# Optimization experiments

Measured on AMD Instinct MI355X. Metric: run time of the kernel, lower is better.

Reference implementation:

```python
import jax, jax.numpy as jnp
import numpy as np

B, NQ, NC, C, NH, NP, DFF, HH, WW = 4, 300, 16, 256, 8, 4, 2048, 128, 128


def _ln(x, g, b):
    m = jnp.mean(x, -1, keepdims=True)
    v = jnp.mean((x - m) ** 2, -1, keepdims=True)
    return (x - m) / jnp.sqrt(v + 1e-5) * g + b


def _mha(x, wi, bi, wo, bo, n_heads):
    Bx, L, Cx = x.shape
    d = Cx // n_heads
    q, k, v = jnp.split(x @ wi.T + bi, 3, axis=-1)
    sh = lambda t: t.reshape(Bx, L, n_heads, d).transpose(0, 2, 1, 3)
    scale = float(1.0 / np.sqrt(d))
    a = jax.nn.softmax(jnp.einsum('bhqd,bhkd->bhqk', sh(q), sh(k)) * scale, axis=-1)
    o = jnp.einsum('bhqk,bhkd->bhqd', a, sh(v)).transpose(0, 2, 1, 3).reshape(Bx, L, Cx)
    return o @ wo.T + bo


def _grid_sample(im, grid):
    # im: [N, Ch, H, W]; grid: [N, L, P, 2] in [-1,1]; bilinear, zeros padding, align_corners=False
    N, Ch, H, W = im.shape
    gx = (grid[..., 0] + 1.0) * (W * 0.5) - 0.5
    gy = (grid[..., 1] + 1.0) * (H * 0.5) - 0.5
    x0 = jnp.floor(gx)
    y0 = jnp.floor(gy)
    wx1 = gx - x0
    wy1 = gy - y0
    imf = im.reshape(N, Ch, H * W)

    def gather(xi, yi):
        valid = ((xi >= 0) & (xi < W) & (yi >= 0) & (yi < H)).astype(im.dtype)
        idx = jnp.clip(yi, 0, H - 1).astype(jnp.int32) * W + jnp.clip(xi, 0, W - 1).astype(jnp.int32)
        vals = jnp.take_along_axis(imf, idx.reshape(N, 1, -1), axis=2).reshape(N, Ch, *xi.shape[1:])
        return vals * valid[:, None]

    return (gather(x0, y0) * ((1 - wx1) * (1 - wy1))[:, None]
            + gather(x0 + 1, y0) * (wx1 * (1 - wy1))[:, None]
            + gather(x0, y0 + 1) * ((1 - wx1) * wy1)[:, None]
            + gather(x0 + 1, y0 + 1) * (wx1 * wy1)[:, None])


def setup_inputs() -> dict:
    key = jax.random.key(0)
    ks = jax.random.split(key, 30)
    s = 0.02
    p = lambda k, shp: jax.random.normal(k, shp, jnp.float32) * s
    cxcy = jax.random.uniform(ks[0], (B, NQ * NC, 2), jnp.float32)
    wh = jax.random.uniform(ks[1], (B, NQ * NC, 2), jnp.float32) * 0.2 + 0.02
    return {
        'inst_query': jax.random.normal(ks[2], (B, NQ, C), jnp.float32),
        'sub_contour_query': jax.random.normal(ks[3], (B, NQ, NC, C), jnp.float32),
        'memory_feats': jax.random.normal(ks[4], (B, HH * WW, C), jnp.float32),
        'reference_boxes': jnp.concatenate([cxcy, wh], axis=-1),
        'inst_in_w': p(ks[5], (3 * C, C)), 'inst_in_b': p(ks[6], (3 * C,)),
        'inst_out_w': p(ks[7], (C, C)), 'inst_out_b': p(ks[8], (C,)),
        'sc_in_w': p(ks[9], (3 * C, C)), 'sc_in_b': p(ks[10], (3 * C,)),
        'sc_out_w': p(ks[11], (C, C)), 'sc_out_b': p(ks[12], (C,)),
        'off_w': p(ks[13], (NH * NP * 2, C)), 'off_b': p(ks[14], (NH * NP * 2,)),
        'aw_w': p(ks[15], (NH * NP, C)), 'aw_b': p(ks[16], (NH * NP,)),
        'outp_w': p(ks[17], (C, C)), 'outp_b': p(ks[18], (C,)),
        'lin1_w': p(ks[19], (DFF, C)), 'lin1_b': p(ks[20], (DFF,)),
        'lin2_w': p(ks[21], (C, DFF)), 'lin2_b': p(ks[22], (C,)),
        'n1_g': jnp.ones((C,), jnp.float32), 'n1_b': jnp.zeros((C,), jnp.float32),
        'n2_g': jnp.ones((C,), jnp.float32), 'n2_b': jnp.zeros((C,), jnp.float32),
        'n3_g': jnp.ones((C,), jnp.float32), 'n3_b': jnp.zeros((C,), jnp.float32),
        'H': HH, 'W': WW,
    }


def reference(inst_query, sub_contour_query, memory_feats, reference_boxes,
              inst_in_w, inst_in_b, inst_out_w, inst_out_b,
              sc_in_w, sc_in_b, sc_out_w, sc_out_b,
              off_w, off_b, aw_w, aw_b, outp_w, outp_b,
              lin1_w, lin1_b, lin2_w, lin2_b,
              n1_g, n1_b, n2_g, n2_b, n3_g, n3_b, H, W):
    Bx, Nq, Nc, Cx = sub_contour_query.shape
    Lq = Nq * Nc
    hd = Cx // NH
    # --- decoupled self-attention (eval mode: dropout = identity) ---
    inst_o = _mha(inst_query, inst_in_w, inst_in_b, inst_out_w, inst_out_b, NH)
    sc = sub_contour_query.transpose(0, 2, 1, 3).reshape(Bx * Nc, Nq, Cx)
    sc_o = _mha(sc, sc_in_w, sc_in_b, sc_out_w, sc_out_b, NH)
    sc_o = sc_o.reshape(Bx, Nc, Nq, Cx).transpose(0, 2, 1, 3)
    q_sa = sc_o + inst_o[:, :, None, :]
    tgt = (sub_contour_query + q_sa).reshape(Bx, Lq, Cx)
    tgt = _ln(tgt + q_sa.reshape(Bx, Lq, Cx), n1_g, n1_b)
    # --- deformable cross-attention ---
    offsets = (tgt @ off_w.T + off_b).reshape(Bx, Lq, NH, NP, 2)
    aw = jax.nn.softmax((tgt @ aw_w.T + aw_b).reshape(Bx, Lq, NH, NP), axis=-1)
    ref = reference_boxes[:, :, None, None, :]
    loc = ref[..., :2] + offsets * ref[..., 2:] * 0.5
    grid = (loc * 2.0 - 1.0).transpose(0, 2, 1, 3, 4).reshape(Bx * NH, Lq, NP, 2)
    mem = memory_feats.reshape(Bx, H, W, Cx).transpose(0, 3, 1, 2).reshape(Bx * NH, hd, H, W)
    samp = _grid_sample(mem, grid).reshape(Bx, NH, hd, Lq, NP).transpose(0, 3, 1, 4, 2)  # [B,Lq,nH,nP,hd]
    tgt2 = (samp * aw[..., None]).sum(3).reshape(Bx, Lq, Cx) @ outp_w.T + outp_b
    tgt = _ln(tgt + tgt2, n2_g, n2_b)
    # --- FFN ---
    tgt2 = jax.nn.relu(tgt @ lin1_w.T + lin1_b) @ lin2_w.T + lin2_b
    tgt = _ln(tgt + tgt2, n3_g, n3_b)
    return tgt.reshape(Bx, Nq, Nc, Cx)
```

## Files before the change

### kernel.cpp

```cpp
#include <hip/hip_runtime.h>
#include <hip/hip_bf16.h>
#include <math.h>


typedef unsigned short u16;
typedef unsigned int u32;
typedef __attribute__((ext_vector_type(4))) float f32x4;
typedef __attribute__((ext_vector_type(8))) short s16x8;

__device__ __forceinline__ float b2f(u16 u) {
    union { u32 u; float f; } v; v.u = ((u32)u) << 16; return v.f;
}
__device__ __forceinline__ u16 f2b(float f) {
    union { float f; u32 u; } v; v.f = f;
    u32 r = v.u + 0x7fffu + ((v.u >> 16) & 1u);
    return (u16)(r >> 16);
}
__device__ __forceinline__ u32 pkbf(float a, float b) {
    u32 r;
    asm("v_cvt_pk_bf16_f32 %0, %1, %2" : "=v"(r) : "v"(a), "v"(b));
    return r;
}

#define GLOAD_LDS16(g, l) \
    __builtin_amdgcn_global_load_lds((const __attribute__((address_space(1))) void*)(g), \
                                     (__attribute__((address_space(3))) void*)(l), 16, 0, 0)

struct CvtSeg { const float* src; u16* dst; int nv; };
struct Cvt8 { CvtSeg s[8]; };

__global__ __launch_bounds__(256) void cvt_multi(Cvt8 a, int totalv) {
    int v = blockIdx.x * 256 + threadIdx.x;
    if (v >= totalv) return;
    int si = 0;
    while (si < 7 && v >= a.s[si].nv) { v -= a.s[si].nv; ++si; }
    const float* src = a.s[si].src + (size_t)v * 8;
    u16* dst = a.s[si].dst + (size_t)v * 8;
    float4 x = *(const float4*)src;
    float4 y = *(const float4*)(src + 4);
    u16 u[8] = { f2b(x.x), f2b(x.y), f2b(x.z), f2b(x.w),
                 f2b(y.x), f2b(y.y), f2b(y.z), f2b(y.w) };
    *(uint4*)dst = *(const uint4*)u;
}

__global__ __launch_bounds__(256) void pack_offaw(
    const float* __restrict__ off_w, const float* __restrict__ off_b,
    const float* __restrict__ aw_w, const float* __restrict__ aw_b,
    u16* __restrict__ wout, float* __restrict__ bout)
{
    int r = blockIdx.x, c = threadIdx.x;
    float v = 0.f;
    if (r < 64) v = off_w[r * 256 + c];
    else if (r < 96) v = aw_w[(r - 64) * 256 + c];
    wout[r * 256 + c] = f2b(v);
    if (c == 0) bout[r] = (r < 64) ? off_b[r] : (r < 96 ? aw_b[r - 64] : 0.f);
}

template<int RELU, int OUTBF16, int TM>
__global__ __launch_bounds__(256) void gemm_mfma(
    const u16* __restrict__ A, const u16* __restrict__ W,
    const float* __restrict__ bias, void* __restrict__ Cout,
    int M, int N, int K)
{
    constexpr int MI = TM / 32;
    constexpr int AU = TM / 64;
    __shared__ u16 smem[TM * 32 + 128 * 32];
    u16* Asm = smem;
    u16* Bsm = smem + TM * 32;
    const int tid = threadIdx.x;
    const int wave = tid >> 6, lane = tid & 63;
    const int bm = blockIdx.y * TM, bn = blockIdx.x * 128;
    const int wr = (wave >> 1) * (TM / 2), wc = (wave & 1) * 64;
    const int fr = lane & 15;
    const int fk = (lane >> 4) * 8;
    f32x4 acc[MI][4] = {};

    for (int k0 = 0; k0 < K; k0 += 32) {
        __syncthreads();
#pragma unroll
        for (int c = 0; c < AU; ++c) {
            int b = (c * 256 + tid) * 16;
            int row = b >> 6;
            int ke = (b & 63) >> 1;
            int ra = bm + row; if (ra >= M) ra = M - 1;
            GLOAD_LDS16(A + (size_t)ra * K + k0 + ke, Asm + (c * 256 + wave * 64) * 8);
        }
#pragma unroll
        for (int c = 0; c < 2; ++c) {
            int b = (c * 256 + tid) * 16;
            int row = b >> 6;
            int ke = (b & 63) >> 1;
            int rb = bn + row;
            GLOAD_LDS16(W + (size_t)rb * K + k0 + ke, Bsm + (c * 256 + wave * 64) * 8);
        }
        __syncthreads();
        s16x8 af[MI], bf[4];
#pragma unroll
        for (int i = 0; i < MI; ++i)
            af[i] = *(const s16x8*)(Asm + (wr + i * 16 + fr) * 32 + fk);
#pragma unroll
        for (int i = 0; i < 4; ++i)
            bf[i] = *(const s16x8*)(Bsm + (wc + i * 16 + fr) * 32 + fk);
#pragma unroll
        for (int mi = 0; mi < MI; ++mi)
#pragma unroll
            for (int ni = 0; ni < 4; ++ni)
                acc[mi][ni] = __builtin_amdgcn_mfma_f32_16x16x32_bf16(
                    af[mi], bf[ni], acc[mi][ni], 0, 0, 0);
    }
    const int cc = lane & 15, cr4 = (lane >> 4) * 4;
    if (OUTBF16) {
#pragma unroll
        for (int p = 0; p < TM / 32; ++p) {
            const int base = p * 32;
            __syncthreads();
#pragma unroll
            for (int mi = 0; mi < MI; ++mi) {
                int rowoff = wr + mi * 16;
                if (rowoff < base || rowoff >= base + 32) continue;
#pragma unroll
                for (int ni = 0; ni < 4; ++ni) {
                    int col = wc + ni * 16 + cc;
                    float bv = bias[bn + col];
#pragma unroll
                    for (int j = 0; j < 4; ++j) {
                        float v = acc[mi][ni][j] + bv;
                        if (RELU) v = fmaxf(v, 0.f);
                        smem[(rowoff - base + cr4 + j) * 136 + col] = f2b(v);
                    }
                }
            }
            __syncthreads();
            for (int t = tid; t < 512; t += 256) {
                int row = t >> 4, ck = t & 15;
                int grow = bm + base + row;
                if (grow < M)
                    *(uint4*)((u16*)Cout + (size_t)grow * N + bn + ck * 8) =
                        *(const uint4*)&smem[row * 136 + ck * 8];
            }
        }
    } else {
#pragma unroll
        for (int mi = 0; mi < MI; ++mi) {
#pragma unroll
            for (int ni = 0; ni < 4; ++ni) {
                int col = bn + wc + ni * 16 + cc;
                float bv = bias[col];
#pragma unroll
                for (int j = 0; j < 4; ++j) {
                    int row = bm + wr + mi * 16 + cr4 + j;
                    if (row >= M) continue;
                    float v = acc[mi][ni][j] + bv;
                    if (RELU) v = fmaxf(v, 0.f);
                    ((float*)Cout)[(size_t)row * N + col] = v;
                }
            }
        }
    }
}

#define VIDX(d, k) ((((k) >> 3) ^ ((d) & 7)) * 8 + ((k) & 7))

__global__ __launch_bounds__(256) void attn_mfma(
    const u16* __restrict__ qkv, u16* __restrict__ O, int S)
{
    const int bh = blockIdx.x / S, seg = blockIdx.x % S;
    const int bi = bh >> 3, h = bh & 7;
    __shared__ u16 Ks[320][40];
    __shared__ u16 Vt[32][384];
    const int tid = threadIdx.x;

    for (int idx = tid; idx < 1200; idx += 256) {
        int k = idx >> 2, sub = idx & 3;
        const u16* kp = qkv + ((size_t)(bi * 300 + k)) * 768 + 256 + h * 32 + sub * 8;
        *(uint4*)&Ks[k][sub * 8] = *(const uint4*)kp;
    }
    for (int idx = tid; idx < 600; idx += 256) {
        int kp2 = idx >> 2, sub = idx & 3;
        int k0 = kp2 * 2;
        const u16* vp = qkv + ((size_t)(bi * 300 + k0)) * 768 + 512 + h * 32 + sub * 8;
        uint4 v0 = *(const uint4*)vp;
        uint4 v1 = *(const uint4*)(vp + 768);
        u16 a0[8], a1[8];
        *(uint4*)a0 = v0; *(uint4*)a1 = v1;
#pragma unroll
        for (int j = 0; j < 8; ++j) {
            int d = sub * 8 + j;
            *(u32*)&Vt[d][VIDX(d, k0)] = (u32)a0[j] | ((u32)a1[j] << 16);
        }
    }
    for (int idx = tid; idx < 320; idx += 256) {
        int d = idx & 31, k0 = 300 + (idx >> 5) * 2;
        *(u32*)&Vt[d][VIDX(d, k0)] = 0;
    }
    __syncthreads();

    const int lane = tid & 63, wave = tid >> 6;
    const int c = lane & 15, g = lane >> 4;
    const int fk = g * 8;
    const f32x4 zero = { 0.f, 0.f, 0.f, 0.f };
    const float SCL2 = 0.25505416f;
    const int sA = c + ((g & 1) << 5);
    const int sB = sA + 16;
    const bool hi = g >= 2;

    for (int qt = seg * 4 + wave; qt < 19; qt += 4 * S) {
        int qrow = qt * 16 + c; if (qrow > 299) qrow = 299;
        s16x8 afq = *(const s16x8*)(qkv + ((size_t)(bi * 300 + qrow)) * 768 + h * 32 + fk);
        f32x4 acc0 = zero, acc1 = zero;
        float m = -1e30f, l = 0.f;

        for (int kc = 0; kc < 10; ++kc) {
            const int kb = kc * 32;
            s16x8 ak0 = *(const s16x8*)&Ks[kb + c][fk];
            s16x8 ak1 = *(const s16x8*)&Ks[kb + 16 + c][fk];
            __builtin_amdgcn_s_setprio(1);
            f32x4 s0 = __builtin_amdgcn_mfma_f32_16x16x32_bf16(ak0, afq, zero, 0, 0, 0);
            f32x4 s1 = __builtin_amdgcn_mfma_f32_16x16x32_bf16(ak1, afq, zero, 0, 0, 0);
            __builtin_amdgcn_s_setprio(0);
            if (kb == 288) {
#pragma unroll
                for (int j = 0; j < 4; ++j) {
                    if (g == 3) s0[j] = -1e30f;
                    s1[j] = -1e30f;
                }
            }
            float cm = fmaxf(fmaxf(fmaxf(s0[0], s0[1]), fmaxf(s0[2], s0[3])),
                             fmaxf(fmaxf(s1[0], s1[1]), fmaxf(s1[2], s1[3])));
            cm = fmaxf(cm, __shfl_xor(cm, 16));
            cm = fmaxf(cm, __shfl_xor(cm, 32));
            float mn = fmaxf(m, cm);
            float corr = exp2f((m - mn) * SCL2);
            m = mn;
            float p0[4], p1[4];
#pragma unroll
            for (int j = 0; j < 4; ++j) {
                p0[j] = exp2f((s0[j] - m) * SCL2);
                p1[j] = exp2f((s1[j] - m) * SCL2);
            }
            float cs = (p0[0] + p0[1]) + (p0[2] + p0[3])
                     + (p1[0] + p1[1]) + (p1[2] + p1[3]);
            cs += __shfl_xor(cs, 16);
            cs += __shfl_xor(cs, 32);
            l = l * corr + cs;
            u32 w0 = pkbf(p0[0], p0[1]), w1 = pkbf(p0[2], p0[3]);
            u32 w2 = pkbf(p1[0], p1[1]), w3 = pkbf(p1[2], p1[3]);
            int x0 = __shfl((int)w0, sA), x1 = __shfl((int)w1, sA);
            int x2 = __shfl((int)w2, sA), x3 = __shfl((int)w3, sA);
            int y0 = __shfl((int)w0, sB), y1 = __shfl((int)w1, sB);
            int y2 = __shfl((int)w2, sB), y3 = __shfl((int)w3, sB);
            union { u32 w[4]; s16x8 v; } afp;
            afp.w[0] = hi ? (u32)x2 : (u32)x0;
            afp.w[1] = hi ? (u32)x3 : (u32)x1;
            afp.w[2] = hi ? (u32)y2 : (u32)y0;
            afp.w[3] = hi ? (u32)y3 : (u32)y1;
            float c0 = __shfl(corr, g * 4 + 0), c1 = __shfl(corr, g * 4 + 1);
            float c2 = __shfl(corr, g * 4 + 2), c3 = __shfl(corr, g * 4 + 3);
            acc0[0] *= c0; acc0[1] *= c1; acc0[2] *= c2; acc0[3] *= c3;
            acc1[0] *= c0; acc1[1] *= c1; acc1[2] *= c2; acc1[3] *= c3;
            s16x8 bv0 = *(const s16x8*)&Vt[c][VIDX(c, kb + fk)];
            s16x8 bv1 = *(const s16x8*)&Vt[16 + c][VIDX(16 + c, kb + fk)];
            __builtin_amdgcn_s_setprio(1);
            acc0 = __builtin_amdgcn_mfma_f32_16x16x32_bf16(afp.v, bv0, acc0, 0, 0, 0);
            acc1 = __builtin_amdgcn_mfma_f32_16x16x32_bf16(afp.v, bv1, acc1, 0, 0, 0);
            __builtin_amdgcn_s_setprio(0);
        }
        float l0 = __shfl(l, g * 4 + 0), l1 = __shfl(l, g * 4 + 1);
        float l2 = __shfl(l, g * 4 + 2), l3 = __shfl(l, g * 4 + 3);
        float lj[4] = { l0, l1, l2, l3 };
#pragma unroll
        for (int j = 0; j < 4; ++j) {
            int q = qt * 16 + g * 4 + j;
            if (q < 300) {
                float r = 1.f / lj[j];
                u16* op = O + ((size_t)(bi * 300 + q)) * 256 + h * 32;
                op[c]      = f2b(acc0[j] * r);
                op[16 + c] = f2b(acc1[j] * r);
            }
        }
    }
}

__global__ __launch_bounds__(256) void sc_transpose(
    const float* __restrict__ scq, u16* __restrict__ out)
{
    int row = blockIdx.x * 4 + (threadIdx.x >> 6);
    int c4 = (threadIdx.x & 63) * 4;
    int b = row / 4800;
    int rem = row % 4800;
    int nc = rem / 300, nq = rem % 300;
    float4 v = *(const float4*)(scq + ((size_t)((b * 300 + nq) * 16 + nc)) * 256 + c4);
    u16 u[4] = { f2b(v.x), f2b(v.y), f2b(v.z), f2b(v.w) };
    *(uint2*)(out + (size_t)row * 256 + c4) = *(const uint2*)u;
}

__global__ __launch_bounds__(256) void ln1_combine(
    const float* __restrict__ scq, const float* __restrict__ sco,
    const float* __restrict__ insto, const float* __restrict__ g,
    const float* __restrict__ bta, float* __restrict__ tgt,
    u16* __restrict__ tgtb)
{
    int row = blockIdx.x * 4 + (threadIdx.x >> 6);
    int c4 = (threadIdx.x & 63) * 4;
    int b = row / 4800;
    int rem = row % 4800;
    int nq = rem >> 4, nc = rem & 15;
    float4 a = *(const float4*)(scq + (size_t)row * 256 + c4);
    float4 s = *(const float4*)(sco + ((size_t)((b * 16 + nc) * 300 + nq)) * 256 + c4);
    float4 i = *(const float4*)(insto + ((size_t)(b * 300 + nq)) * 256 + c4);
    float4 v = { a.x + 2.f * (s.x + i.x), a.y + 2.f * (s.y + i.y),
                 a.z + 2.f * (s.z + i.z), a.w + 2.f * (s.w + i.w) };
    float sm = v.x + v.y + v.z + v.w;
    float s2 = v.x * v.x + v.y * v.y + v.z * v.z + v.w * v.w;
#pragma unroll
    for (int o = 32; o; o >>= 1) { sm += __shfl_xor(sm, o); s2 += __shfl_xor(s2, o); }
    float mean = sm * (1.f / 256.f);
    float rstd = 1.f / sqrtf(s2 * (1.f / 256.f) - mean * mean + 1e-5f);
    float4 gv = *(const float4*)(g + c4);
    float4 bv = *(const float4*)(bta + c4);
    float4 r = { (v.x - mean) * rstd * gv.x + bv.x, (v.y - mean) * rstd * gv.y + bv.y,
                 (v.z - mean) * rstd * gv.z + bv.z, (v.w - mean) * rstd * gv.w + bv.w };
    *(float4*)(tgt + (size_t)row * 256 + c4) = r;
    u16 u[4] = { f2b(r.x), f2b(r.y), f2b(r.z), f2b(r.w) };
    *(uint2*)(tgtb + (size_t)row * 256 + c4) = *(const uint2*)u;
}

__global__ __launch_bounds__(256) void ln_add(
    const float* __restrict__ x, const float* __restrict__ y,
    const float* __restrict__ g, const float* __restrict__ bta,
    float* __restrict__ dst, u16* __restrict__ bdst)
{
    int row = blockIdx.x * 4 + (threadIdx.x >> 6);
    int c4 = (threadIdx.x & 63) * 4;
    float4 a = *(const float4*)(x + (size_t)row * 256 + c4);
    float4 b = *(const float4*)(y + (size_t)row * 256 + c4);
    float4 v = { a.x + b.x, a.y + b.y, a.z + b.z, a.w + b.w };
    float sm = v.x + v.y + v.z + v.w;
    float s2 = v.x * v.x + v.y * v.y + v.z * v.z + v.w * v.w;
#pragma unroll
    for (int o = 32; o; o >>= 1) { sm += __shfl_xor(sm, o); s2 += __shfl_xor(s2, o); }
    float mean = sm * (1.f / 256.f);
    float rstd = 1.f / sqrtf(s2 * (1.f / 256.f) - mean * mean + 1e-5f);
    float4 gv = *(const float4*)(g + c4);
    float4 bv = *(const float4*)(bta + c4);
    float4 r = { (v.x - mean) * rstd * gv.x + bv.x, (v.y - mean) * rstd * gv.y + bv.y,
                 (v.z - mean) * rstd * gv.z + bv.z, (v.w - mean) * rstd * gv.w + bv.w };
    *(float4*)(dst + (size_t)row * 256 + c4) = r;
    if (bdst) {
        u16 u[4] = { f2b(r.x), f2b(r.y), f2b(r.z), f2b(r.w) };
        *(uint2*)(bdst + (size_t)row * 256 + c4) = *(const uint2*)u;
    }
}

__global__ __launch_bounds__(256) void deform_sample(
    const float* __restrict__ oaw, const float* __restrict__ refb,
    const float* __restrict__ mem, u16* __restrict__ samp)
{
    const int row = blockIdx.x;
    const int b = row / 4800;
    const int tid = threadIdx.x;
    const int h = tid >> 5;
    const float4 rb = *(const float4*)(refb + (size_t)row * 4);
    const float* base = oaw + (size_t)row * 128;
    float a0 = base[64 + h * 4 + 0], a1 = base[64 + h * 4 + 1];
    float a2 = base[64 + h * 4 + 2], a3 = base[64 + h * 4 + 3];
    float am = fmaxf(fmaxf(a0, a1), fmaxf(a2, a3));
    float e0 = __expf(a0 - am), e1 = __expf(a1 - am), e2 = __expf(a2 - am), e3 = __expf(a3 - am);
    float rs = 1.f / (e0 + e1 + e2 + e3);
    float wp[4] = { e0 * rs, e1 * rs, e2 * rs, e3 * rs };
    const float* op = base + h * 8;
    const float* mb = mem + (size_t)b * 16384 * 256 + tid;

    int offs[16];
    float wts[16];
#pragma unroll
    for (int p = 0; p < 4; ++p) {
        float gx = (rb.x + op[p * 2 + 0] * rb.z * 0.5f) * 128.f - 0.5f;
        float gy = (rb.y + op[p * 2 + 1] * rb.w * 0.5f) * 128.f - 0.5f;
        float x0f = floorf(gx), y0f = floorf(gy);
        int x0 = (int)x0f, y0 = (int)y0f;
        float wx1 = gx - x0f, wy1 = gy - y0f;
        float wx0 = 1.f - wx1, wy0 = 1.f - wy1;
        float vx0 = ((unsigned)x0 < 128u) ? 1.f : 0.f;
        float vx1 = ((unsigned)(x0 + 1) < 128u) ? 1.f : 0.f;
        float vy0 = ((unsigned)y0 < 128u) ? 1.f : 0.f;
        float vy1 = ((unsigned)(y0 + 1) < 128u) ? 1.f : 0.f;
        int xc0 = min(max(x0, 0), 127), xc1 = min(max(x0 + 1, 0), 127);
        int yc0 = min(max(y0, 0), 127), yc1 = min(max(y0 + 1, 0), 127);
        offs[p * 4 + 0] = (yc0 * 128 + xc0) << 8;
        offs[p * 4 + 1] = (yc0 * 128 + xc1) << 8;
        offs[p * 4 + 2] = (yc1 * 128 + xc0) << 8;
        offs[p * 4 + 3] = (yc1 * 128 + xc1) << 8;
        wts[p * 4 + 0] = wp[p] * wx0 * wy0 * vx0 * vy0;
        wts[p * 4 + 1] = wp[p] * wx1 * wy0 * vx1 * vy0;
        wts[p * 4 + 2] = wp[p] * wx0 * wy1 * vx0 * vy1;
        wts[p * 4 + 3] = wp[p] * wx1 * wy1 * vx1 * vy1;
    }
    float vals[16];
#pragma unroll
    for (int i = 0; i < 16; ++i) vals[i] = mb[offs[i]];
    float acc = 0.f;
#pragma unroll
    for (int i = 0; i < 16; ++i) acc = fmaf(vals[i], wts[i], acc);
    samp[(size_t)row * 256 + tid] = f2b(acc);
}

extern "C" void kernel_launch(void* const* d_in, const int* in_sizes, int n_in,
                              void* d_out, int out_size, void* d_ws, size_t ws_size,
                              hipStream_t stream) {
    const float* inst_query = (const float*)d_in[0];
    const float* sub_contour = (const float*)d_in[1];
    const float* memory_feats = (const float*)d_in[2];
    const float* ref_boxes = (const float*)d_in[3];
    const float* inst_in_w = (const float*)d_in[4];
    const float* inst_in_b = (const float*)d_in[5];
    const float* inst_out_w = (const float*)d_in[6];
    const float* inst_out_b = (const float*)d_in[7];
    const float* sc_in_w = (const float*)d_in[8];
    const float* sc_in_b = (const float*)d_in[9];
    const float* sc_out_w = (const float*)d_in[10];
    const float* sc_out_b = (const float*)d_in[11];
    const float* off_w = (const float*)d_in[12];
    const float* off_b = (const float*)d_in[13];
    const float* aw_w = (const float*)d_in[14];
    const float* aw_b = (const float*)d_in[15];
    const float* outp_w = (const float*)d_in[16];
    const float* outp_b = (const float*)d_in[17];
    const float* lin1_w = (const float*)d_in[18];
    const float* lin1_b = (const float*)d_in[19];
    const float* lin2_w = (const float*)d_in[20];
    const float* lin2_b = (const float*)d_in[21];
    const float* n1_g = (const float*)d_in[22];
    const float* n1_b = (const float*)d_in[23];
    const float* n2_g = (const float*)d_in[24];
    const float* n2_b = (const float*)d_in[25];
    const float* n3_g = (const float*)d_in[26];
    const float* n3_b = (const float*)d_in[27];

    u16* wsb = (u16*)d_ws;
    u16* qkv_b   = wsb;
    u16* xbuf_b  = qkv_b + 14745600;
    u16* obuf_b  = xbuf_b + 4915200;
    u16* tgt_b   = obuf_b + 4915200;
    u16* w_inst_in  = tgt_b + 4915200;
    u16* w_inst_out = w_inst_in + 196608;
    u16* w_sc_in    = w_inst_out + 65536;
    u16* w_sc_out   = w_sc_in + 196608;
    u16* w_outp     = w_sc_out + 65536;
    u16* w_lin1     = w_outp + 65536;
    u16* w_lin2     = w_lin1 + 524288;
    u16* w_offaw    = w_lin2 + 524288;
    u16* ffn1_b = qkv_b;
    u16* instq_b = tgt_b;
    float* fp    = (float*)(w_offaw + 32768);
    float* insto = fp;
    float* tgt   = insto + 307200;
    float* t2    = tgt + 4915200;
    float* oawb  = t2 + 4915200;
    float* b_offaw = oawb + 2457600;
    size_t base_bytes = (size_t)((char*)(b_offaw + 128) - (char*)d_ws);
    size_t ffn_off = (base_bytes + 255) & ~(size_t)255;
    u16* ffn1_full = (u16*)((char*)d_ws + ffn_off);
    bool full_ffn = ws_size >= ffn_off + (size_t)2 * 19200 * 2048;

    dim3 blk(256);

    Cvt8 ca;
    ca.s[0] = { inst_in_w,  w_inst_in,  196608 / 8 };
    ca.s[1] = { inst_out_w, w_inst_out, 65536 / 8 };
    ca.s[2] = { sc_in_w,    w_sc_in,    196608 / 8 };
    ca.s[3] = { sc_out_w,   w_sc_out,   65536 / 8 };
    ca.s[4] = { outp_w,     w_outp,     65536 / 8 };
    ca.s[5] = { lin1_w,     w_lin1,     524288 / 8 };
    ca.s[6] = { lin2_w,     w_lin2,     524288 / 8 };
    ca.s[7] = { inst_query, instq_b,    307200 / 8 };
    int totalv = (196608 * 2 + 65536 * 3 + 524288 * 2 + 307200) / 8;
    cvt_multi<<<(totalv + 255) / 256, blk, 0, stream>>>(ca, totalv);
    pack_offaw<<<128, blk, 0, stream>>>(off_w, off_b, aw_w, aw_b, w_offaw, b_offaw);

    gemm_mfma<0,1,128><<<dim3(6, 10), blk, 0, stream>>>(instq_b, w_inst_in, inst_in_b, qkv_b, 1200, 768, 256);
    attn_mfma<<<128, blk, 0, stream>>>(qkv_b, obuf_b, 4);
    gemm_mfma<0,0,64><<<dim3(2, 19), blk, 0, stream>>>(obuf_b, w_inst_out, inst_out_b, insto, 1200, 256, 256);
    sc_transpose<<<4800, blk, 0, stream>>>(sub_contour, xbuf_b);
    gemm_mfma<0,1,128><<<dim3(6, 150), blk, 0, stream>>>(xbuf_b, w_sc_in, sc_in_b, qkv_b, 19200, 768, 256);
    attn_mfma<<<1024, blk, 0, stream>>>(qkv_b, obuf_b, 2);
    gemm_mfma<0,0,64><<<dim3(2, 300), blk, 0, stream>>>(obuf_b, w_sc_out, sc_out_b, t2, 19200, 256, 256);
    ln1_combine<<<4800, blk, 0, stream>>>(sub_contour, t2, insto, n1_g, n1_b, tgt, tgt_b);
    gemm_mfma<0,0,64><<<dim3(1, 300), blk, 0, stream>>>(tgt_b, w_offaw, b_offaw, oawb, 19200, 128, 256);
    deform_sample<<<19200, blk, 0, stream>>>(oawb, ref_boxes, memory_feats, obuf_b);
    gemm_mfma<0,0,64><<<dim3(2, 300), blk, 0, stream>>>(obuf_b, w_outp, outp_b, t2, 19200, 256, 256);
    ln_add<<<4800, blk, 0, stream>>>(tgt, t2, n2_g, n2_b, tgt, tgt_b);
    if (full_ffn) {
        gemm_mfma<1,1,128><<<dim3(16, 150), blk, 0, stream>>>(tgt_b, w_lin1, lin1_b, ffn1_full, 19200, 2048, 256);
        gemm_mfma<0,0,64><<<dim3(2, 300), blk, 0, stream>>>(ffn1_full, w_lin2, lin2_b, t2, 19200, 256, 2048);
    } else {
        for (int c = 0; c < 2; ++c) {
            gemm_mfma<1,1,128><<<dim3(16, 75), blk, 0, stream>>>(tgt_b + (size_t)c * 9600 * 256, w_lin1, lin1_b, ffn1_b, 9600, 2048, 256);
            gemm_mfma<0,0,64><<<dim3(2, 150), blk, 0, stream>>>(ffn1_b, w_lin2, lin2_b, t2 + (size_t)c * 9600 * 256, 9600, 256, 2048);
        }
    }
    ln_add<<<4800, blk, 0, stream>>>(tgt, t2, n3_g, n3_b, (float*)d_out, nullptr);
}
```

Measured before the change: 339.8 us.

## Double-buffer GEMM LDS tiles with async prefetch and direct bf16 epilogue

The bf16 MFMA GEMM now keeps two LDS buffers and issues the global-to-LDS loads for the next K tile before computing on the current one. It uses explicit vmcnt waits and raw s_barrier in place of the two __syncthreads per iteration. The bf16 output path also drops the LDS-staged, coalesced uint4 store and writes scattered 2-byte values straight from registers, which removes the epilogue barriers but may reduce store coalescing. LDS use doubles, which can lower occupancy.

```diff
diff --git a/kernel.cpp b/kernel.cpp
--- a/kernel.cpp
+++ b/kernel.cpp
@@ -64,9 +64,9 @@
 {
     constexpr int MI = TM / 32;
     constexpr int AU = TM / 64;
-    __shared__ u16 smem[TM * 32 + 128 * 32];
-    u16* Asm = smem;
-    u16* Bsm = smem + TM * 32;
+    constexpr int NLD = AU + 2;
+    constexpr int BUFE = TM * 32 + 128 * 32;
+    __shared__ u16 smem[2 * BUFE];
     const int tid = threadIdx.x;
     const int wave = tid >> 6, lane = tid & 63;
     const int bm = blockIdx.y * TM, bn = blockIdx.x * 128;
@@ -75,8 +75,9 @@
     const int fk = (lane >> 4) * 8;
     f32x4 acc[MI][4] = {};
 
-    for (int k0 = 0; k0 < K; k0 += 32) {
-        __syncthreads();
+    auto stage = [&](int buf, int k0) {
+        u16* Asm = smem + buf * BUFE;
+        u16* Bsm = Asm + TM * 32;
 #pragma unroll
         for (int c = 0; c < AU; ++c) {
             int b = (c * 256 + tid) * 16;
@@ -93,7 +94,22 @@
             int rb = bn + row;
             GLOAD_LDS16(W + (size_t)rb * K + k0 + ke, Bsm + (c * 256 + wave * 64) * 8);
         }
-        __syncthreads();
+    };
+
+    stage(0, 0);
+    int cur = 0;
+    for (int k0 = 0; k0 < K; k0 += 32) {
+        if (k0 + 32 < K) {
+            stage(cur ^ 1, k0 + 32);
+            if constexpr (NLD == 3) asm volatile("s_waitcnt vmcnt(3)" ::: "memory");
+            else                    asm volatile("s_waitcnt vmcnt(4)" ::: "memory");
+        } else {
+            asm volatile("s_waitcnt vmcnt(0)" ::: "memory");
+        }
+        __builtin_amdgcn_sched_barrier(0);
+        __builtin_amdgcn_s_barrier();
+        const u16* Asm = smem + cur * BUFE;
+        const u16* Bsm = Asm + TM * 32;
         s16x8 af[MI], bf[4];
 #pragma unroll
         for (int i = 0; i < MI; ++i)
@@ -107,53 +123,25 @@
             for (int ni = 0; ni < 4; ++ni)
                 acc[mi][ni] = __builtin_amdgcn_mfma_f32_16x16x32_bf16(
                     af[mi], bf[ni], acc[mi][ni], 0, 0, 0);
+        __builtin_amdgcn_sched_barrier(0);
+        __builtin_amdgcn_s_barrier();
+        cur ^= 1;
     }
     const int cc = lane & 15, cr4 = (lane >> 4) * 4;
-    if (OUTBF16) {
-#pragma unroll
-        for (int p = 0; p < TM / 32; ++p) {
-            const int base = p * 32;
-            __syncthreads();
-#pragma unroll
-            for (int mi = 0; mi < MI; ++mi) {
-                int rowoff = wr + mi * 16;
-                if (rowoff < base || rowoff >= base + 32) continue;
-#pragma unroll
-                for (int ni = 0; ni < 4; ++ni) {
-                    int col = wc + ni * 16 + cc;
-                    float bv = bias[bn + col];
-#pragma unroll
-                    for (int j = 0; j < 4; ++j) {
-                        float v = acc[mi][ni][j] + bv;
-                        if (RELU) v = fmaxf(v, 0.f);
-                        smem[(rowoff - base + cr4 + j) * 136 + col] = f2b(v);
-                    }
-                }
-            }
-            __syncthreads();
-            for (int t = tid; t < 512; t += 256) {
-                int row = t >> 4, ck = t & 15;
-                int grow = bm + base + row;
-                if (grow < M)
-                    *(uint4*)((u16*)Cout + (size_t)grow * N + bn + ck * 8) =
-                        *(const uint4*)&smem[row * 136 + ck * 8];
-            }
-        }
-    } else {
-#pragma unroll
-        for (int mi = 0; mi < MI; ++mi) {
-#pragma unroll
-            for (int ni = 0; ni < 4; ++ni) {
-                int col = bn + wc + ni * 16 + cc;
-                float bv = bias[col];
-#pragma unroll
-                for (int j = 0; j < 4; ++j) {
-                    int row = bm + wr + mi * 16 + cr4 + j;
-                    if (row >= M) continue;
-                    float v = acc[mi][ni][j] + bv;
-                    if (RELU) v = fmaxf(v, 0.f);
-                    ((float*)Cout)[(size_t)row * N + col] = v;
-                }
+#pragma unroll
+    for (int mi = 0; mi < MI; ++mi) {
+#pragma unroll
+        for (int ni = 0; ni < 4; ++ni) {
+            int col = bn + wc + ni * 16 + cc;
+            float bv = bias[col];
+#pragma unroll
+            for (int j = 0; j < 4; ++j) {
+                int row = bm + wr + mi * 16 + cr4 + j;
+                if (row >= M) continue;
+                float v = acc[mi][ni][j] + bv;
+                if (RELU) v = fmaxf(v, 0.f);
+                if (OUTBF16) ((u16*)Cout)[(size_t)row * N + col] = f2b(v);
+                else ((float*)Cout)[(size_t)row * N + col] = v;
             }
         }
     }
```

Result: slower. 349.3 us (+2.8%).
